# Performance work log

Hardware: AMD Instinct MI355X
Metric: run time of the kernel (lower is better)

Reference implementation:

```python
import jax, jax.numpy as jnp
import numpy as np

B, T, D, H = 4, 2048, 1024, 16
DH = D // H


def setup_inputs() -> dict:
    key = jax.random.key(0)
    ks = jax.random.split(key, 7)
    s = 1.0 / np.sqrt(D)
    inp = {
        "query": jax.random.normal(ks[0], (B, T, D), jnp.float32),
        "key": jax.random.normal(ks[1], (B, T, D), jnp.float32),
        "value": jax.random.normal(ks[2], (B, T, D), jnp.float32),
        "wq": jax.random.normal(ks[3], (D, D), jnp.float32) * s,
        "wk": jax.random.normal(ks[4], (D, D), jnp.float32) * s,
        "wv": jax.random.normal(ks[5], (D, D), jnp.float32) * s,
        "wo": jax.random.normal(ks[6], (D, D), jnp.float32) * s,
    }
    # additive causal mask, broadcast over batch and heads
    neg = jnp.finfo(jnp.float32).min
    causal = jnp.where(jnp.tril(jnp.ones((T, T), bool)), 0.0, neg)
    inp["attn_mask"] = causal[None, None, :, :].astype(jnp.float32)
    return inp


def _split_heads(x):
    # [B, T, D] -> [B, H, T, DH]
    Bx, Tx, _ = x.shape
    return x.reshape(Bx, Tx, H, DH).transpose(0, 2, 1, 3)


def reference(query, key, value, attn_mask, wq, wk, wv, wo):
    # nn.Linear(bias=False): y = x @ W^T
    q = _split_heads(query @ wq.T)
    k = _split_heads(key @ wk.T)
    v = _split_heads(value @ wv.T)
    scale = 1.0 / jnp.sqrt(jnp.asarray(DH, q.dtype))
    scores = jnp.einsum("bhqd,bhkd->bhqk", q, k) * scale + attn_mask
    weights = jax.nn.softmax(scores, axis=-1)
    out = jnp.einsum("bhqk,bhkd->bhqd", weights, v)
    out = out.transpose(0, 2, 1, 3).reshape(query.shape[0], query.shape[1], D)
    out = out @ wo.T
    return out, k, v
```

## Files before the change

kernel.cpp:

```cpp
#include <hip/hip_runtime.h>
#include <hip/hip_bf16.h>
#include <math.h>

constexpr int Mdim = 8192;
constexpr int Ndim = 1024;
constexpr int Kdim = 1024;
constexpr int Tseq = 2048;
constexpr int NH   = 16;

typedef __attribute__((ext_vector_type(8))) short short8;
typedef __attribute__((ext_vector_type(4))) float floatx4;

__device__ __forceinline__ unsigned short f2b(float f) {
  unsigned int x = __builtin_bit_cast(unsigned int, f);
  x += 0x7fffu + ((x >> 16) & 1u);
  return (unsigned short)(x >> 16);
}
__device__ __forceinline__ unsigned int pk2(float a, float b) {
  unsigned int ua = __builtin_bit_cast(unsigned int, a) + 0x8000u;
  unsigned int ub = __builtin_bit_cast(unsigned int, b) + 0x8000u;
  return (ua >> 16) | (ub & 0xffff0000u);
}
__device__ __forceinline__ void gld16(const void* g, const void* l) {
  __builtin_amdgcn_global_load_lds(
      (const __attribute__((address_space(1))) unsigned int*)(unsigned long long)g,
      (__attribute__((address_space(3))) unsigned int*)(unsigned int)(unsigned long long)l,
      16, 0, 0);
}
__device__ __forceinline__ void barrier_raw() {
  __builtin_amdgcn_sched_barrier(0);
  __builtin_amdgcn_s_barrier();
  __builtin_amdgcn_sched_barrier(0);
}

__global__ __launch_bounds__(256) void cast_k(
    const float* __restrict__ q, const float* __restrict__ k,
    const float* __restrict__ v, const float* __restrict__ wq,
    const float* __restrict__ wk, const float* __restrict__ wv,
    const float* __restrict__ wo,
    unsigned short* d0, unsigned short* d1, unsigned short* d2,
    unsigned short* d3, unsigned short* d4, unsigned short* d5,
    unsigned short* d6) {
  int y = blockIdx.y;
  const float* s = y == 0 ? q : y == 1 ? k : y == 2 ? v
                 : y == 3 ? wq : y == 4 ? wk : y == 5 ? wv : wo;
  unsigned short* d = y == 0 ? d0 : y == 1 ? d1 : y == 2 ? d2
                    : y == 3 ? d3 : y == 4 ? d4 : y == 5 ? d5 : d6;
  size_t n = (y < 3) ? (size_t)Mdim * Kdim : (size_t)Ndim * Kdim;
  size_t i = ((size_t)blockIdx.x * 256 + threadIdx.x) * 8;
  if (i >= n) return;
  float4 a = *(const float4*)(s + i);
  float4 b = *(const float4*)(s + i + 4);
  uint4 w;
  w.x = (unsigned)f2b(a.x) | ((unsigned)f2b(a.y) << 16);
  w.y = (unsigned)f2b(a.z) | ((unsigned)f2b(a.w) << 16);
  w.z = (unsigned)f2b(b.x) | ((unsigned)f2b(b.y) << 16);
  w.w = (unsigned)f2b(b.z) | ((unsigned)f2b(b.w) << 16);
  *(uint4*)(d + i) = w;
}

__launch_bounds__(512, 2)
__global__ void gemm_qkv(const unsigned short* __restrict__ Aq,
                         const unsigned short* __restrict__ Ak,
                         const unsigned short* __restrict__ Av,
                         const unsigned short* __restrict__ Wq,
                         const unsigned short* __restrict__ Wk,
                         const unsigned short* __restrict__ Wv,
                         unsigned short* __restrict__ Qh,
                         unsigned short* __restrict__ Kh,
                         float* __restrict__ Kout,
                         unsigned short* __restrict__ VTg,
                         float* __restrict__ Vout) {
  __shared__ __align__(16) unsigned short As[2][2][8192];
  __shared__ __align__(16) unsigned short Bs[2][2][8192];

  const int z = blockIdx.z;
  const unsigned short* __restrict__ A = z == 0 ? Aq : z == 1 ? Ak : Av;
  const unsigned short* __restrict__ W = z == 0 ? Wq : z == 1 ? Wk : Wv;

  const int tid  = threadIdx.x;
  const int lane = tid & 63;
  const int wave = tid >> 6;
  const int mw   = wave >> 2;
  const int nw   = wave & 3;
  const int l15  = lane & 15;
  const int quad = lane >> 4;
  const int sw   = l15 & 7;

  const int flat = blockIdx.y * 4 + blockIdx.x;
  const int swz  = (flat & 7) * 16 + (flat >> 3);
  const int m0   = (swz >> 2) * 256;
  const int n0   = (swz & 3) * 256;

  const int srow8 = lane >> 3;
  const int sg    = lane & 7;

  floatx4 acc[2][2][4][2];
#pragma unroll
  for (int a0 = 0; a0 < 2; a0++)
#pragma unroll
    for (int b0 = 0; b0 < 2; b0++)
#pragma unroll
      for (int c0 = 0; c0 < 4; c0++)
#pragma unroll
        for (int d0 = 0; d0 < 2; d0++) acc[a0][b0][c0][d0] = (floatx4)0.0f;

  auto stage = [&](const unsigned short* __restrict__ S, int rb, int kt,
                   unsigned short* dst) {
#pragma unroll
    for (int h = 0; h < 2; h++)
#pragma unroll
      for (int j = 0; j < 2; j++) {
        int c = wave * 2 + j;
        int r = c * 8 + srow8;
        int G = sg ^ (r & 7);
        gld16(S + (size_t)(rb + h * 128 + r) * Kdim + kt + G * 8,
              dst + h * 8192 + c * 512);
      }
  };
  auto ldA = [&](int par, int mh, short8 (&a)[4][2]) {
    const unsigned short* base = &As[par][mw][0];
#pragma unroll
    for (int mi = 0; mi < 4; mi++) {
      const unsigned short* rp = base + (mh * 64 + mi * 16 + l15) * 64;
#pragma unroll
      for (int ks = 0; ks < 2; ks++)
        a[mi][ks] = *(const short8*)(rp + (((ks * 4 + quad) ^ sw) << 3));
    }
  };
  auto ldB = [&](int par, int nh, short8 (&b)[2][2]) {
    const unsigned short* base = &Bs[par][nw >> 1][0];
#pragma unroll
    for (int ni = 0; ni < 2; ni++) {
      const unsigned short* rp =
          base + ((nw & 1) * 64 + nh * 32 + ni * 16 + l15) * 64;
#pragma unroll
      for (int ks = 0; ks < 2; ks++)
        b[ni][ks] = *(const short8*)(rp + (((ks * 4 + quad) ^ sw) << 3));
    }
  };
  auto mmaq = [&](floatx4 (&c)[4][2], short8 (&a)[4][2], short8 (&b)[2][2]) {
    __builtin_amdgcn_s_setprio(1);
#pragma unroll
    for (int mi = 0; mi < 4; mi++)
#pragma unroll
      for (int ni = 0; ni < 2; ni++)
#pragma unroll
        for (int ks = 0; ks < 2; ks++)
          c[mi][ni] = __builtin_amdgcn_mfma_f32_16x16x32_bf16(
              b[ni][ks], a[mi][ks], c[mi][ni], 0, 0, 0);
    __builtin_amdgcn_s_setprio(0);
  };

  stage(A, m0, 0, &As[0][0][0]);
  stage(W, n0, 0, &Bs[0][0][0]);
  stage(A, m0, 64, &As[1][0][0]);
  stage(W, n0, 64, &Bs[1][0][0]);
  __builtin_amdgcn_sched_barrier(0);
  asm volatile("s_waitcnt vmcnt(8)");
  barrier_raw();

  short8 a[4][2], b0[2][2], b1[2][2];
  constexpr int NT = Kdim / 64;
  for (int t = 0; t < NT; ++t) {
    const int par = t & 1;
    const int ktn = (t + 2) * 64;
    ldA(par, 0, a);
    ldB(par, 0, b0);
    barrier_raw();
    mmaq(acc[0][0], a, b0);
    barrier_raw();
    ldB(par, 1, b1);
    barrier_raw();
    mmaq(acc[0][1], a, b1);
    barrier_raw();
    ldA(par, 1, a);
    if (t < NT - 2) stage(W, n0, ktn, &Bs[par][0][0]);
    barrier_raw();
    mmaq(acc[1][0], a, b0);
    barrier_raw();
    if (t < NT - 2) stage(A, m0, ktn, &As[par][0][0]);
    barrier_raw();
    mmaq(acc[1][1], a, b1);
    __builtin_amdgcn_sched_barrier(0);
    if (t < NT - 2)
      asm volatile("s_waitcnt vmcnt(8)");
    else if (t == NT - 2)
      asm volatile("s_waitcnt vmcnt(0)");
    barrier_raw();
  }

  const int gmb = m0 + mw * 128;
  const int gnb = n0 + nw * 64;
#pragma unroll
  for (int mh = 0; mh < 2; mh++)
#pragma unroll
    for (int mi = 0; mi < 4; mi++) {
      int t_abs = gmb + mh * 64 + mi * 16 + l15;
      int b = t_abs >> 11, tb = t_abs & (Tseq - 1);
#pragma unroll
      for (int nh = 0; nh < 2; nh++)
#pragma unroll
        for (int ni = 0; ni < 2; ni++) {
          int gn0 = gnb + nh * 32 + ni * 16 + quad * 4;
          int h = gn0 >> 6, dh0 = gn0 & 63;
          size_t base = ((size_t)((b * NH + h) * Tseq + tb)) * 64 + dh0;
          floatx4 v = acc[mh][nh][mi][ni];
          if (z == 0) {
            ushort4 w = {f2b(v[0]), f2b(v[1]), f2b(v[2]), f2b(v[3])};
            *(ushort4*)(Qh + base) = w;
          } else if (z == 1) {
            *(float4*)(Kout + base) = *(float4*)&v;
            ushort4 w = {f2b(v[0]), f2b(v[1]), f2b(v[2]), f2b(v[3])};
            *(ushort4*)(Kh + base) = w;
          } else {
            *(float4*)(Vout + base) = *(float4*)&v;
            size_t vtb = ((size_t)((b * NH + h) * 64 + dh0)) * Tseq + tb;
#pragma unroll
            for (int r = 0; r < 4; r++)
              VTg[vtb + (size_t)r * Tseq] = f2b(v[r]);
          }
        }
    }
}

__launch_bounds__(256)
__global__ void gemm_o(const unsigned short* __restrict__ A,
                       const unsigned short* __restrict__ W,
                       float* __restrict__ Cf) {
  __shared__ __align__(16) unsigned short As[128 * 64];
  __shared__ __align__(16) unsigned short Bs[128 * 64];

  const int tid  = threadIdx.x;
  const int lane = tid & 63;
  const int wave = tid >> 6;
  const int l15  = lane & 15;
  const int quad = lane >> 4;
  const int sw   = l15 & 7;
  const int m0 = blockIdx.y * 128;
  const int n0 = blockIdx.x * 128;
  const int wm = (wave >> 1) * 64;
  const int wn = (wave & 1) * 64;

  floatx4 acc[4][4];
  for (int i = 0; i < 4; i++)
    for (int j = 0; j < 4; j++) acc[i][j] = (floatx4)0.0f;

  const int srow8 = lane >> 3;
  const int sg    = lane & 7;

  for (int kt = 0; kt < Kdim; kt += 64) {
    for (int jj = 0; jj < 4; jj++) {
      int cc = wave * 4 + jj;
      int row = cc * 8 + srow8;
      int G = sg ^ (row & 7);
      gld16(A + (size_t)(m0 + row) * Kdim + kt + G * 8, As + cc * 512);
      gld16(W + (size_t)(n0 + row) * Kdim + kt + G * 8, Bs + cc * 512);
    }
    __syncthreads();

    for (int hf = 0; hf < 2; hf++) {
      short8 af[4], bw[4];
      for (int mi = 0; mi < 4; mi++)
        af[mi] = *(const short8*)(As + (wm + mi * 16 + l15) * 64 +
                                  (((hf * 4 + quad) ^ sw) << 3));
      for (int ni = 0; ni < 4; ni++)
        bw[ni] = *(const short8*)(Bs + (wn + ni * 16 + l15) * 64 +
                                  (((hf * 4 + quad) ^ sw) << 3));
      for (int mi = 0; mi < 4; mi++)
        for (int ni = 0; ni < 4; ni++)
          acc[mi][ni] = __builtin_amdgcn_mfma_f32_16x16x32_bf16(
              bw[ni], af[mi], acc[mi][ni], 0, 0, 0);
    }
    __syncthreads();
  }

  for (int mi = 0; mi < 4; mi++) {
    int t_abs = m0 + wm + mi * 16 + l15;
    for (int ni = 0; ni < 4; ni++) {
      int gn0 = n0 + wn + ni * 16 + quad * 4;
      floatx4 v = acc[mi][ni];
      *(float4*)(Cf + (size_t)t_abs * Ndim + gn0) = *(float4*)&v;
    }
  }
}

__launch_bounds__(256)
__global__ void attn_k(const unsigned short* __restrict__ Qh,
                       const unsigned short* __restrict__ Kh,
                       const unsigned short* __restrict__ VTg,
                       unsigned short* __restrict__ Og) {
  __shared__ __align__(16) unsigned short Kt[2][64 * 64];
  __shared__ __align__(16) unsigned short Vt[2][64 * 64];
  __shared__ __align__(16) unsigned short Pl[64 * 64];

  const int tid  = threadIdx.x;
  const int lane = tid & 63;
  const int wave = tid >> 6;
  const int l15  = lane & 15;
  const int quad = lane >> 4;
  const int sw   = l15 & 7;
  const int bh   = blockIdx.x;

  const size_t headoff = (size_t)bh * Tseq * 64;
  const int srow8 = lane >> 3;
  const int sg    = lane & 7;
  const float kscale = 0.18033688011112042f;
  const int b = bh >> 4, h = bh & 15;

  for (int half = 0; half < 2; half++) {
    const int a   = half ? blockIdx.y : 31 - blockIdx.y;
    const int nkt = a + 1;
    const int qg  = a * 64 + wave * 16 + l15;

    short8 bq[2];
#pragma unroll
    for (int hf = 0; hf < 2; hf++)
      bq[hf] = *(const short8*)(Qh + headoff + (size_t)qg * 64 +
                                hf * 32 + quad * 8);

    floatx4 o[4];
#pragma unroll
    for (int nb = 0; nb < 4; nb++) o[nb] = (floatx4)0.0f;
    float mrow = -INFINITY, lrow = 0.0f;

    auto stage = [&](int par, int kt) {
      const int k0 = kt * 64;
#pragma unroll
      for (int jj = 0; jj < 2; jj++) {
        int cc  = wave * 2 + jj;
        int row = cc * 8 + srow8;
        int G   = sg ^ (row & 7);
        gld16(Kh + headoff + (size_t)(k0 + row) * 64 + G * 8,
              &Kt[par][cc * 512]);
        gld16(VTg + ((size_t)bh * 64 + row) * Tseq + k0 + G * 8,
              &Vt[par][cc * 512]);
      }
    };

    stage(0, 0);
    __builtin_amdgcn_sched_barrier(0);
    asm volatile("s_waitcnt vmcnt(0)");
    barrier_raw();

    for (int kt = 0; kt < nkt; kt++) {
      const int par = kt & 1;
      if (kt + 1 < nkt) stage(par ^ 1, kt + 1);
      const int k0 = kt * 64;

      floatx4 st[4];
#pragma unroll
      for (int nb = 0; nb < 4; nb++) {
        const unsigned short* kr = &Kt[par][(nb * 16 + l15) * 64];
        short8 ak0 = *(const short8*)(kr + ((quad ^ sw) << 3));
        short8 ak1 = *(const short8*)(kr + (((quad + 4) ^ sw) << 3));
        floatx4 acc0 = (floatx4)0.0f;
        acc0 = __builtin_amdgcn_mfma_f32_16x16x32_bf16(ak0, bq[0], acc0, 0, 0, 0);
        acc0 = __builtin_amdgcn_mfma_f32_16x16x32_bf16(ak1, bq[1], acc0, 0, 0, 0);
        st[nb] = acc0;
      }

      if (kt == nkt - 1) {
#pragma unroll
        for (int nb = 0; nb < 4; nb++)
#pragma unroll
          for (int r = 0; r < 4; r++) {
            int kg = k0 + nb * 16 + quad * 4 + r;
            if (kg > qg) st[nb][r] = -INFINITY;
          }
      }

      float mt = fmaxf(fmaxf(st[0][0], st[0][1]), fmaxf(st[0][2], st[0][3]));
#pragma unroll
      for (int nb = 1; nb < 4; nb++)
        mt = fmaxf(mt, fmaxf(fmaxf(st[nb][0], st[nb][1]),
                             fmaxf(st[nb][2], st[nb][3])));
      mt = fmaxf(mt, __shfl_xor(mt, 16, 64));
      mt = fmaxf(mt, __shfl_xor(mt, 32, 64));

      if (!__all((mt - mrow) * kscale <= 8.0f)) {
        float mnew = fmaxf(mrow, mt);
        float al = __builtin_amdgcn_exp2f((mrow - mnew) * kscale);
        mrow = mnew;
        lrow *= al;
#pragma unroll
        for (int nb = 0; nb < 4; nb++)
#pragma unroll
          for (int r = 0; r < 4; r++) o[nb][r] *= al;
      }
      const float ms = mrow * kscale;

      float rs = 0.0f;
      const int prow = (wave * 16 + l15) * 64;
#pragma unroll
      for (int nb = 0; nb < 4; nb++) {
        float p0 = __builtin_amdgcn_exp2f(__builtin_fmaf(st[nb][0], kscale, -ms));
        float p1 = __builtin_amdgcn_exp2f(__builtin_fmaf(st[nb][1], kscale, -ms));
        float p2 = __builtin_amdgcn_exp2f(__builtin_fmaf(st[nb][2], kscale, -ms));
        float p3 = __builtin_amdgcn_exp2f(__builtin_fmaf(st[nb][3], kscale, -ms));
        rs += (p0 + p1) + (p2 + p3);
        uint2 w = {pk2(p0, p1), pk2(p2, p3)};
        int klb = nb * 16 + quad * 4;
        int colp = (((klb >> 3) ^ sw) << 3) | (klb & 7);
        *(uint2*)(Pl + prow + colp) = w;
      }
      rs += __shfl_xor(rs, 16, 64);
      rs += __shfl_xor(rs, 32, 64);
      lrow += rs;

      short8 av[4][2];
#pragma unroll
      for (int nb = 0; nb < 4; nb++) {
        const unsigned short* vr = &Vt[par][(nb * 16 + l15) * 64];
        av[nb][0] = *(const short8*)(vr + ((quad ^ sw) << 3));
        av[nb][1] = *(const short8*)(vr + (((quad + 4) ^ sw) << 3));
      }
      const unsigned short* pr = Pl + prow;
      short8 bp0 = *(const short8*)(pr + ((quad ^ sw) << 3));
      short8 bp1 = *(const short8*)(pr + (((quad + 4) ^ sw) << 3));
#pragma unroll
      for (int nb = 0; nb < 4; nb++) {
        o[nb] = __builtin_amdgcn_mfma_f32_16x16x32_bf16(av[nb][0], bp0, o[nb], 0, 0, 0);
        o[nb] = __builtin_amdgcn_mfma_f32_16x16x32_bf16(av[nb][1], bp1, o[nb], 0, 0, 0);
      }

      __builtin_amdgcn_sched_barrier(0);
      asm volatile("s_waitcnt vmcnt(0)");
      barrier_raw();
    }

    float inv = 1.0f / lrow;
    size_t rowoff = ((size_t)(b * Tseq + qg)) * 1024 + h * 64;
#pragma unroll
    for (int nb = 0; nb < 4; nb++) {
      ushort4 w;
      w.x = f2b(o[nb][0] * inv);
      w.y = f2b(o[nb][1] * inv);
      w.z = f2b(o[nb][2] * inv);
      w.w = f2b(o[nb][3] * inv);
      *(ushort4*)(Og + rowoff + nb * 16 + quad * 4) = w;
    }
  }
}

extern "C" void kernel_launch(void* const* d_in, const int* in_sizes, int n_in,
                              void* d_out, int out_size, void* d_ws, size_t ws_size,
                              hipStream_t stream) {
  const float* q  = (const float*)d_in[0];
  const float* k  = (const float*)d_in[1];
  const float* v  = (const float*)d_in[2];
  const float* wq = (const float*)d_in[3];
  const float* wk = (const float*)d_in[4];
  const float* wv = (const float*)d_in[5];
  const float* wo = (const float*)d_in[6];
  float* out = (float*)d_out;

  constexpr size_t BTD = (size_t)Mdim * Kdim;
  constexpr size_t DD  = (size_t)Ndim * Kdim;
  constexpr size_t MB16 = BTD * 2;

  char* ws = (char*)d_ws;
  unsigned short* Qh  = (unsigned short*)(ws);
  unsigned short* Kh  = (unsigned short*)(ws + MB16);
  unsigned short* VTg = (unsigned short*)(ws + 2 * MB16);
  unsigned short* Og  = (unsigned short*)(ws + 3 * MB16);
  unsigned short* qb  = (unsigned short*)(ws + 4 * MB16);
  unsigned short* kb  = (unsigned short*)(ws + 5 * MB16);
  unsigned short* vb  = (unsigned short*)(ws + 6 * MB16);
  unsigned short* wqb = (unsigned short*)(ws + 7 * MB16);
  unsigned short* wkb = wqb + DD;
  unsigned short* wvb = wkb + DD;
  unsigned short* wob = wvb + DD;

  float* Kout = out + BTD;
  float* Vout = out + 2 * BTD;

  cast_k<<<dim3(4096, 7), 256, 0, stream>>>(q, k, v, wq, wk, wv, wo,
                                            qb, kb, vb, wqb, wkb, wvb, wob);

  gemm_qkv<<<dim3(Ndim / 256, Mdim / 256, 3), 512, 0, stream>>>(
      qb, kb, vb, wqb, wkb, wvb, Qh, Kh, Kout, VTg, Vout);

  attn_k<<<dim3(4 * NH, 16), 256, 0, stream>>>(Qh, Kh, VTg, Og);

  gemm_o<<<dim3(Ndim / 128, Mdim / 128), 256, 0, stream>>>(Og, wob, out);
}
```

Baseline: 366.5 us.

## Replace pipelined 256x256 QKV GEMM with simple 128x128 tile kernel

The QKV projection GEMM drops its 512-thread, 256x256-tile, double-buffered LDS pipeline with interleaved barriers. It now uses the simpler 128x128, 256-thread, single-buffer loop already used by the output-projection GEMM, with a remapped block order that swizzles workgroups across the three projections. This raises the block count and occupancy (launch bounds 256,4) but loses the overlap of global loads with MFMA and halves per-tile data reuse.

```diff
diff --git a/kernel.cpp b/kernel.cpp
--- a/kernel.cpp
+++ b/kernel.cpp
@@ -59,7 +59,7 @@
   *(uint4*)(d + i) = w;
 }
 
-__launch_bounds__(512, 2)
+__launch_bounds__(256, 4)
 __global__ void gemm_qkv(const unsigned short* __restrict__ Aq,
                          const unsigned short* __restrict__ Ak,
                          const unsigned short* __restrict__ Av,
@@ -71,165 +71,18 @@
                          float* __restrict__ Kout,
                          unsigned short* __restrict__ VTg,
                          float* __restrict__ Vout) {
-  __shared__ __align__(16) unsigned short As[2][2][8192];
-  __shared__ __align__(16) unsigned short Bs[2][2][8192];
-
-  const int z = blockIdx.z;
+  __shared__ __align__(16) unsigned short As[128 * 64];
+  __shared__ __align__(16) unsigned short Bs[128 * 64];
+
+  const int flat = (blockIdx.z * 64 + blockIdx.y) * 8 + blockIdx.x;
+  const int wgid = (flat & 7) * 192 + (flat >> 3);
+  const int z    = wgid >> 9;
+  const int rem  = wgid & 511;
+  const int m0   = (rem >> 3) * 128;
+  const int n0   = (rem & 7) * 128;
+
   const unsigned short* __restrict__ A = z == 0 ? Aq : z == 1 ? Ak : Av;
   const unsigned short* __restrict__ W = z == 0 ? Wq : z == 1 ? Wk : Wv;
-
-  const int tid  = threadIdx.x;
-  const int lane = tid & 63;
-  const int wave = tid >> 6;
-  const int mw   = wave >> 2;
-  const int nw   = wave & 3;
-  const int l15  = lane & 15;
-  const int quad = lane >> 4;
-  const int sw   = l15 & 7;
-
-  const int flat = blockIdx.y * 4 + blockIdx.x;
-  const int swz  = (flat & 7) * 16 + (flat >> 3);
-  const int m0   = (swz >> 2) * 256;
-  const int n0   = (swz & 3) * 256;
-
-  const int srow8 = lane >> 3;
-  const int sg    = lane & 7;
-
-  floatx4 acc[2][2][4][2];
-#pragma unroll
-  for (int a0 = 0; a0 < 2; a0++)
-#pragma unroll
-    for (int b0 = 0; b0 < 2; b0++)
-#pragma unroll
-      for (int c0 = 0; c0 < 4; c0++)
-#pragma unroll
-        for (int d0 = 0; d0 < 2; d0++) acc[a0][b0][c0][d0] = (floatx4)0.0f;
-
-  auto stage = [&](const unsigned short* __restrict__ S, int rb, int kt,
-                   unsigned short* dst) {
-#pragma unroll
-    for (int h = 0; h < 2; h++)
-#pragma unroll
-      for (int j = 0; j < 2; j++) {
-        int c = wave * 2 + j;
-        int r = c * 8 + srow8;
-        int G = sg ^ (r & 7);
-        gld16(S + (size_t)(rb + h * 128 + r) * Kdim + kt + G * 8,
-              dst + h * 8192 + c * 512);
-      }
-  };
-  auto ldA = [&](int par, int mh, short8 (&a)[4][2]) {
-    const unsigned short* base = &As[par][mw][0];
-#pragma unroll
-    for (int mi = 0; mi < 4; mi++) {
-      const unsigned short* rp = base + (mh * 64 + mi * 16 + l15) * 64;
-#pragma unroll
-      for (int ks = 0; ks < 2; ks++)
-        a[mi][ks] = *(const short8*)(rp + (((ks * 4 + quad) ^ sw) << 3));
-    }
-  };
-  auto ldB = [&](int par, int nh, short8 (&b)[2][2]) {
-    const unsigned short* base = &Bs[par][nw >> 1][0];
-#pragma unroll
-    for (int ni = 0; ni < 2; ni++) {
-      const unsigned short* rp =
-          base + ((nw & 1) * 64 + nh * 32 + ni * 16 + l15) * 64;
-#pragma unroll
-      for (int ks = 0; ks < 2; ks++)
-        b[ni][ks] = *(const short8*)(rp + (((ks * 4 + quad) ^ sw) << 3));
-    }
-  };
-  auto mmaq = [&](floatx4 (&c)[4][2], short8 (&a)[4][2], short8 (&b)[2][2]) {
-    __builtin_amdgcn_s_setprio(1);
-#pragma unroll
-    for (int mi = 0; mi < 4; mi++)
-#pragma unroll
-      for (int ni = 0; ni < 2; ni++)
-#pragma unroll
-        for (int ks = 0; ks < 2; ks++)
-          c[mi][ni] = __builtin_amdgcn_mfma_f32_16x16x32_bf16(
-              b[ni][ks], a[mi][ks], c[mi][ni], 0, 0, 0);
-    __builtin_amdgcn_s_setprio(0);
-  };
-
-  stage(A, m0, 0, &As[0][0][0]);
-  stage(W, n0, 0, &Bs[0][0][0]);
-  stage(A, m0, 64, &As[1][0][0]);
-  stage(W, n0, 64, &Bs[1][0][0]);
-  __builtin_amdgcn_sched_barrier(0);
-  asm volatile("s_waitcnt vmcnt(8)");
-  barrier_raw();
-
-  short8 a[4][2], b0[2][2], b1[2][2];
-  constexpr int NT = Kdim / 64;
-  for (int t = 0; t < NT; ++t) {
-    const int par = t & 1;
-    const int ktn = (t + 2) * 64;
-    ldA(par, 0, a);
-    ldB(par, 0, b0);
-    barrier_raw();
-    mmaq(acc[0][0], a, b0);
-    barrier_raw();
-    ldB(par, 1, b1);
-    barrier_raw();
-    mmaq(acc[0][1], a, b1);
-    barrier_raw();
-    ldA(par, 1, a);
-    if (t < NT - 2) stage(W, n0, ktn, &Bs[par][0][0]);
-    barrier_raw();
-    mmaq(acc[1][0], a, b0);
-    barrier_raw();
-    if (t < NT - 2) stage(A, m0, ktn, &As[par][0][0]);
-    barrier_raw();
-    mmaq(acc[1][1], a, b1);
-    __builtin_amdgcn_sched_barrier(0);
-    if (t < NT - 2)
-      asm volatile("s_waitcnt vmcnt(8)");
-    else if (t == NT - 2)
-      asm volatile("s_waitcnt vmcnt(0)");
-    barrier_raw();
-  }
-
-  const int gmb = m0 + mw * 128;
-  const int gnb = n0 + nw * 64;
-#pragma unroll
-  for (int mh = 0; mh < 2; mh++)
-#pragma unroll
-    for (int mi = 0; mi < 4; mi++) {
-      int t_abs = gmb + mh * 64 + mi * 16 + l15;
-      int b = t_abs >> 11, tb = t_abs & (Tseq - 1);
-#pragma unroll
-      for (int nh = 0; nh < 2; nh++)
-#pragma unroll
-        for (int ni = 0; ni < 2; ni++) {
-          int gn0 = gnb + nh * 32 + ni * 16 + quad * 4;
-          int h = gn0 >> 6, dh0 = gn0 & 63;
-          size_t base = ((size_t)((b * NH + h) * Tseq + tb)) * 64 + dh0;
-          floatx4 v = acc[mh][nh][mi][ni];
-          if (z == 0) {
-            ushort4 w = {f2b(v[0]), f2b(v[1]), f2b(v[2]), f2b(v[3])};
-            *(ushort4*)(Qh + base) = w;
-          } else if (z == 1) {
-            *(float4*)(Kout + base) = *(float4*)&v;
-            ushort4 w = {f2b(v[0]), f2b(v[1]), f2b(v[2]), f2b(v[3])};
-            *(ushort4*)(Kh + base) = w;
-          } else {
-            *(float4*)(Vout + base) = *(float4*)&v;
-            size_t vtb = ((size_t)((b * NH + h) * 64 + dh0)) * Tseq + tb;
-#pragma unroll
-            for (int r = 0; r < 4; r++)
-              VTg[vtb + (size_t)r * Tseq] = f2b(v[r]);
-          }
-        }
-    }
-}
-
-__launch_bounds__(256)
-__global__ void gemm_o(const unsigned short* __restrict__ A,
-                       const unsigned short* __restrict__ W,
-                       float* __restrict__ Cf) {
-  __shared__ __align__(16) unsigned short As[128 * 64];
-  __shared__ __align__(16) unsigned short Bs[128 * 64];
 
   const int tid  = threadIdx.x;
   const int lane = tid & 63;
@@ -237,8 +90,6 @@
   const int l15  = lane & 15;
   const int quad = lane >> 4;
   const int sw   = l15 & 7;
-  const int m0 = blockIdx.y * 128;
-  const int n0 = blockIdx.x * 128;
   const int wm = (wave >> 1) * 64;
   const int wn = (wave & 1) * 64;
 
@@ -275,6 +126,83 @@
     __syncthreads();
   }
 
+  const int gm = m0 + wm + l15;
+  for (int mi = 0; mi < 4; mi++) {
+    int t_abs = gm + mi * 16;
+    int b = t_abs >> 11, tb = t_abs & (Tseq - 1);
+    for (int ni = 0; ni < 4; ni++) {
+      int gn0 = n0 + wn + ni * 16 + quad * 4;
+      int h = gn0 >> 6, dh0 = gn0 & 63;
+      size_t base = ((size_t)((b * NH + h) * Tseq + tb)) * 64 + dh0;
+      floatx4 v = acc[mi][ni];
+      if (z == 0) {
+        ushort4 w = {f2b(v[0]), f2b(v[1]), f2b(v[2]), f2b(v[3])};
+        *(ushort4*)(Qh + base) = w;
+      } else if (z == 1) {
+        *(float4*)(Kout + base) = *(float4*)&v;
+        ushort4 w = {f2b(v[0]), f2b(v[1]), f2b(v[2]), f2b(v[3])};
+        *(ushort4*)(Kh + base) = w;
+      } else {
+        *(float4*)(Vout + base) = *(float4*)&v;
+        size_t vtb = ((size_t)((b * NH + h) * 64 + dh0)) * Tseq + tb;
+        for (int r = 0; r < 4; r++)
+          VTg[vtb + (size_t)r * Tseq] = f2b(v[r]);
+      }
+    }
+  }
+}
+
+__launch_bounds__(256)
+__global__ void gemm_o(const unsigned short* __restrict__ A,
+                       const unsigned short* __restrict__ W,
+                       float* __restrict__ Cf) {
+  __shared__ __align__(16) unsigned short As[128 * 64];
+  __shared__ __align__(16) unsigned short Bs[128 * 64];
+
+  const int tid  = threadIdx.x;
+  const int lane = tid & 63;
+  const int wave = tid >> 6;
+  const int l15  = lane & 15;
+  const int quad = lane >> 4;
+  const int sw   = l15 & 7;
+  const int m0 = blockIdx.y * 128;
+  const int n0 = blockIdx.x * 128;
+  const int wm = (wave >> 1) * 64;
+  const int wn = (wave & 1) * 64;
+
+  floatx4 acc[4][4];
+  for (int i = 0; i < 4; i++)
+    for (int j = 0; j < 4; j++) acc[i][j] = (floatx4)0.0f;
+
+  const int srow8 = lane >> 3;
+  const int sg    = lane & 7;
+
+  for (int kt = 0; kt < Kdim; kt += 64) {
+    for (int jj = 0; jj < 4; jj++) {
+      int cc = wave * 4 + jj;
+      int row = cc * 8 + srow8;
+      int G = sg ^ (row & 7);
+      gld16(A + (size_t)(m0 + row) * Kdim + kt + G * 8, As + cc * 512);
+      gld16(W + (size_t)(n0 + row) * Kdim + kt + G * 8, Bs + cc * 512);
+    }
+    __syncthreads();
+
+    for (int hf = 0; hf < 2; hf++) {
+      short8 af[4], bw[4];
+      for (int mi = 0; mi < 4; mi++)
+        af[mi] = *(const short8*)(As + (wm + mi * 16 + l15) * 64 +
+                                  (((hf * 4 + quad) ^ sw) << 3));
+      for (int ni = 0; ni < 4; ni++)
+        bw[ni] = *(const short8*)(Bs + (wn + ni * 16 + l15) * 64 +
+                                  (((hf * 4 + quad) ^ sw) << 3));
+      for (int mi = 0; mi < 4; mi++)
+        for (int ni = 0; ni < 4; ni++)
+          acc[mi][ni] = __builtin_amdgcn_mfma_f32_16x16x32_bf16(
+              bw[ni], af[mi], acc[mi][ni], 0, 0, 0);
+    }
+    __syncthreads();
+  }
+
   for (int mi = 0; mi < 4; mi++) {
     int t_abs = m0 + wm + mi * 16 + l15;
     for (int ni = 0; ni < 4; ni++) {
@@ -478,7 +406,7 @@
   cast_k<<<dim3(4096, 7), 256, 0, stream>>>(q, k, v, wq, wk, wv, wo,
                                             qb, kb, vb, wqb, wkb, wvb, wob);
 
-  gemm_qkv<<<dim3(Ndim / 256, Mdim / 256, 3), 512, 0, stream>>>(
+  gemm_qkv<<<dim3(8, 64, 3), 256, 0, stream>>>(
       qb, kb, vb, wqb, wkb, wvb, Qh, Kh, Kout, VTg, Vout);
 
   attn_k<<<dim3(4 * NH, 16), 256, 0, stream>>>(Qh, Kh, VTg, Og);
```

Result: no change. 366.2 us (-0.1%).
